# Kernel optimization log

Hardware: AMD Instinct MI355X
Metric: run time of the kernel (lower is better)

Reference implementation:

```python
import jax, jax.numpy as jnp
import numpy as np

BATCH = 16384
NUM_CLASSES = 1000
FEA_DIM = 1024
MARGIN = 5.0


def setup_inputs() -> dict:
    key = jax.random.key(0)
    k1, k2, k3 = jax.random.split(key, 3)
    x = jax.random.normal(k1, (BATCH, FEA_DIM), dtype=jnp.float32)
    labels = jax.random.randint(k2, (BATCH,), 0, NUM_CLASSES)
    centers = jax.random.normal(k3, (NUM_CLASSES, FEA_DIM), dtype=jnp.float32)
    return {"x": x, "labels": labels, "centers": centers}


def reference(x, labels, centers):
    # Half squared euclidean distances via the GEMM expansion:
    # 0.5*||a-b||^2 = 0.5*(||a||^2 + ||b||^2 - 2 a.b)
    B = x.shape[0]
    C = centers.shape[0]
    x2 = jnp.sum(x * x, axis=1, keepdims=True)          # [B,1]
    c2 = jnp.sum(centers * centers, axis=1)             # [C]
    d_xc = 0.5 * (x2 + c2[None, :] - 2.0 * (x @ centers.T))   # [B,C]
    d_cc = 0.5 * (c2[:, None] + c2[None, :] - 2.0 * (centers @ centers.T))  # [C,C]

    is_label = labels[:, None] == jnp.arange(C)[None, :]  # [B,C] bool
    inf = jnp.float32(jnp.inf)

    # pos_center: distance to own class center
    pos = jnp.take_along_axis(d_xc, labels[:, None], axis=1)[:, 0]       # [B]
    # neg_center: min distance to any other class center
    neg = jnp.min(jnp.where(is_label, inf, d_xc), axis=1)                # [B]
    # centers term: min distance between own center and any other center
    cen = jnp.min(jnp.where(is_label, inf, d_cc[labels]), axis=1)        # [B]

    loss = jax.nn.relu(pos + MARGIN - neg) + jax.nn.relu(MARGIN + 2.0 - cen)
    return jnp.sum(loss) / B
```

## Files before the change

### kernel.cpp

```cpp
#include <hip/hip_runtime.h>
#include <hip/hip_bf16.h>
#include <stdint.h>

#define BATCH   16384
#define NCLASS  1000
#define CPAD    1024
#define FDIM    1024
#define MARGINF 5.0f

typedef __attribute__((ext_vector_type(4))) float f32x4;
typedef __attribute__((ext_vector_type(8))) short bf16x8;

#define SB()    __builtin_amdgcn_s_barrier()
#define LGKM0() asm volatile("s_waitcnt lgkmcnt(0)" ::: "memory")
#define VMC4()  asm volatile("s_waitcnt vmcnt(4)" ::: "memory")
#define VMC0()  asm volatile("s_waitcnt vmcnt(0)" ::: "memory")
#define SCH0()  __builtin_amdgcn_sched_barrier(0)

__device__ __forceinline__ void gload16(const void* g, void* l) {
    __builtin_amdgcn_global_load_lds(
        (const __attribute__((address_space(1))) void*)g,
        (__attribute__((address_space(3))) void*)l, 16, 0, 0);
}

__device__ __forceinline__ unsigned short f2bf(float f) {
    __hip_bfloat16 h = __float2bfloat16(f);
    return __builtin_bit_cast(unsigned short, h);
}

__global__ void prep(const float* __restrict__ x, const float* __restrict__ c,
                     unsigned short* __restrict__ xb, unsigned short* __restrict__ cb,
                     float* __restrict__ c2, float* __restrict__ out) {
    const int bid = blockIdx.x;
    const int t   = threadIdx.x;
    if (bid == 0 && t == 0) atomicExch(out, 0.0f);
    if (bid < CPAD) {
        const int k = bid;
        if (k >= NCLASS) {
            ((ushort4*)(cb + (size_t)k * FDIM))[t] = make_ushort4(0, 0, 0, 0);
            if (t == 0) c2[k] = 1e30f;
            return;
        }
        float4 v = ((const float4*)(c + (size_t)k * FDIM))[t];
        ushort4 o;
        o.x = f2bf(v.x); o.y = f2bf(v.y); o.z = f2bf(v.z); o.w = f2bf(v.w);
        ((ushort4*)(cb + (size_t)k * FDIM))[t] = o;
        float ss = v.x * v.x + v.y * v.y + v.z * v.z + v.w * v.w;
        #pragma unroll
        for (int s = 1; s < 64; s <<= 1) ss += __shfl_xor(ss, s, 64);
        __shared__ float sred[4];
        int lane = t & 63, wid = t >> 6;
        if (lane == 0) sred[wid] = ss;
        __syncthreads();
        if (t == 0) c2[k] = sred[0] + sred[1] + sred[2] + sred[3];
    } else {
        int i = (bid - CPAD) * 256 + t;
        const int stride = 2048 * 256;
        #pragma unroll
        for (int it = 0; it < 8; ++it, i += stride) {
            float4 v = ((const float4*)x)[i];
            ushort4 o;
            o.x = f2bf(v.x); o.y = f2bf(v.y); o.z = f2bf(v.z); o.w = f2bf(v.w);
            ((ushort4*)xb)[i] = o;
        }
    }
}

__launch_bounds__(256)
__global__ void cc_gemm(const unsigned short* __restrict__ cb,
                        const float* __restrict__ c2,
                        float* __restrict__ cpmin)
{
    __shared__ __align__(16) char sA[128 * 64 * 2];
    __shared__ __align__(16) char sB[128 * 64 * 2];
    const int bid = blockIdx.x;
    const int bx = bid & 7, by = bid >> 3;
    const int t    = threadIdx.x;
    const int lane = t & 63;
    const int wave = t >> 6;
    const int wrow = wave >> 1, wcol = wave & 1;
    const int lo4  = lane & 15, hi2 = lane >> 4;
    const int rowBase = bx * 128, colBase = by * 128;

    f32x4 acc[4][4];
    #pragma unroll
    for (int m = 0; m < 4; m++)
        #pragma unroll
        for (int n = 0; n < 4; n++) acc[m][n] = (f32x4){0.f, 0.f, 0.f, 0.f};

    const int g_t = t & 7, r_t = t >> 3;
    const unsigned short* ga[4]; const unsigned short* gb[4];
    char* la[4]; char* lb[4];
    #pragma unroll
    for (int cch = 0; cch < 4; ++cch) {
        const int row = cch * 32 + r_t;
        const int sc  = g_t ^ (row & 7);
        ga[cch] = cb + (size_t)(rowBase + row) * FDIM + sc * 8;
        gb[cch] = cb + (size_t)(colBase + row) * FDIM + sc * 8;
        la[cch] = sA + (cch * 256 + (t & 192)) * 16;
        lb[cch] = sB + (cch * 256 + (t & 192)) * 16;
    }
    for (int kt = 0; kt < 16; ++kt) {
        __syncthreads();
        #pragma unroll
        for (int cch = 0; cch < 4; ++cch) {
            gload16(ga[cch], la[cch]);
            gload16(gb[cch], lb[cch]);
            ga[cch] += 64; gb[cch] += 64;
        }
        __syncthreads();
        #pragma unroll
        for (int ks = 0; ks < 2; ++ks) {
            bf16x8 af[4], bfr[4];
            #pragma unroll
            for (int m = 0; m < 4; m++) {
                const int r = wrow * 64 + m * 16 + lo4;
                const int slot = (ks * 4 + hi2) ^ (r & 7);
                af[m] = *(const bf16x8*)(sA + r * 128 + slot * 16);
            }
            #pragma unroll
            for (int n = 0; n < 4; n++) {
                const int r = wcol * 64 + n * 16 + lo4;
                const int slot = (ks * 4 + hi2) ^ (r & 7);
                bfr[n] = *(const bf16x8*)(sB + r * 128 + slot * 16);
            }
            #pragma unroll
            for (int m = 0; m < 4; m++)
                #pragma unroll
                for (int n = 0; n < 4; n++)
                    acc[m][n] = __builtin_amdgcn_mfma_f32_16x16x32_bf16(af[m], bfr[n], acc[m][n], 0, 0, 0);
        }
    }
    __syncthreads();
    float* sPM = (float*)sA;
    float bias[4]; int colg[4];
    #pragma unroll
    for (int n = 0; n < 4; n++) {
        const int col = colBase + wcol * 64 + n * 16 + lo4;
        colg[n] = col;
        bias[n] = 0.5f * c2[col];
    }
    #pragma unroll
    for (int m = 0; m < 4; m++) {
        #pragma unroll
        for (int j = 0; j < 4; j++) {
            const int rloc  = wrow * 64 + m * 16 + hi2 * 4 + j;
            const int rglob = rowBase + rloc;
            float vmin = 1e30f;
            #pragma unroll
            for (int n = 0; n < 4; n++) {
                float tv = acc[m][n][j] + bias[n];
                if (colg[n] == rglob) tv = 1e30f;
                vmin = fminf(vmin, tv);
            }
            vmin = fminf(vmin, __shfl_xor(vmin, 1, 64));
            vmin = fminf(vmin, __shfl_xor(vmin, 2, 64));
            vmin = fminf(vmin, __shfl_xor(vmin, 4, 64));
            vmin = fminf(vmin, __shfl_xor(vmin, 8, 64));
            if (lo4 == 0) sPM[wcol * 128 + rloc] = vmin;
        }
    }
    __syncthreads();
    if (t < 128)
        cpmin[(size_t)(rowBase + t) * 8 + by] = fminf(sPM[t], sPM[128 + t]);
}

__launch_bounds__(512, 2)
__global__ void gemm8(const unsigned short* __restrict__ xb,
                      const unsigned short* __restrict__ cb,
                      const float* __restrict__ c2,
                      const int* __restrict__ labels,
                      float* __restrict__ pmin,
                      float* __restrict__ pos)
{
    __shared__ __align__(16) char L[131072];

    const int bid = blockIdx.x;
    const int tid = (bid & 7) * 32 + (bid >> 3);
    const int bx = tid >> 2, by = tid & 3;
    const int rowBase = bx * 256, colBase = by * 256;

    const int t    = threadIdx.x;
    const int lane = t & 63;
    const int w    = t >> 6;
    const int wrow = w >> 2, wcol = w & 3;
    const int lo4  = lane & 15, hi2 = lane >> 4;
    const int wb   = w << 10;

    const int srow = t >> 2;
    const int g0   = (t & 3) ^ (srow & 3);
    const unsigned short* sApt[2];
    const unsigned short* sBpt[2];
    sApt[0] = xb + (size_t)(rowBase + srow)       * FDIM + g0 * 8;
    sApt[1] = xb + (size_t)(rowBase + 128 + srow) * FDIM + g0 * 8;
    sBpt[0] = cb + (size_t)(colBase + srow)       * FDIM + g0 * 8;
    sBpt[1] = cb + (size_t)(colBase + 128 + srow) * FDIM + g0 * 8;

    auto stage = [&](int ldsOff, const unsigned short* s0, const unsigned short* s1) {
        gload16(s0, L + ldsOff + wb);
        gload16(s1, L + ldsOff + 8192 + wb);
    };

    const int gsw = ((hi2 ^ (lo4 & 3)) << 4);
    auto LDA = [&](int slot, int ks, int m) -> bf16x8 {
        const int r = wrow * 128 + m * 16 + lo4;
        return *(const bf16x8*)(L + slot + ks * 16384 + r * 64 + gsw);
    };
    auto LDB = [&](int slot, int ks, int n) -> bf16x8 {
        const int r = wcol * 64 + n * 16 + lo4;
        return *(const bf16x8*)(L + slot + 32768 + ks * 16384 + r * 64 + gsw);
    };

    f32x4 acc[8][4];
    #pragma unroll
    for (int m = 0; m < 8; m++)
        #pragma unroll
        for (int n = 0; n < 4; n++) acc[m][n] = (f32x4){0.f, 0.f, 0.f, 0.f};

    bf16x8 af[8], b0, b1;

#define MFMA16(N0, N1, B0_, B1_)                                                   \
    __builtin_amdgcn_s_setprio(1);                                                 \
    _Pragma("unroll")                                                              \
    for (int m = 0; m < 8; ++m) {                                                  \
        acc[m][N0] = __builtin_amdgcn_mfma_f32_16x16x32_bf16(af[m], B0_, acc[m][N0], 0, 0, 0); \
        acc[m][N1] = __builtin_amdgcn_mfma_f32_16x16x32_bf16(af[m], B1_, acc[m][N1], 0, 0, 0); \
    }                                                                              \
    __builtin_amdgcn_s_setprio(0);

    stage(0,         sApt[0],      sApt[1]);
    stage(32768,     sBpt[0],      sBpt[1]);
    stage(16384,     sApt[0] + 32, sApt[1] + 32);
    stage(49152,     sBpt[0] + 32, sBpt[1] + 32);
    VMC0();
    SB();

    for (int kt = 0; kt < 15; ++kt) {
        const int slot  = (kt & 1) << 16;
        const int nslot = slot ^ 65536;
        const int nk = (kt + 1) * 64;
        #pragma unroll
        for (int m = 0; m < 8; ++m) af[m] = LDA(slot, 0, m);
        b0 = LDB(slot, 0, 0); b1 = LDB(slot, 0, 1);
        stage(nslot, sApt[0] + nk, sApt[1] + nk);
        SB(); LGKM0(); SCH0();
        MFMA16(0, 1, b0, b1);
        SB();
        b0 = LDB(slot, 0, 2); b1 = LDB(slot, 0, 3);
        stage(nslot + 32768, sBpt[0] + nk, sBpt[1] + nk);
        SB(); LGKM0(); SCH0();
        MFMA16(2, 3, b0, b1);
        VMC4();
        SB();
        #pragma unroll
        for (int m = 0; m < 8; ++m) af[m] = LDA(slot, 1, m);
        b0 = LDB(slot, 1, 0); b1 = LDB(slot, 1, 1);
        stage(nslot + 16384, sApt[0] + nk + 32, sApt[1] + nk + 32);
        SB(); LGKM0(); SCH0();
        MFMA16(0, 1, b0, b1);
        SB();
        b0 = LDB(slot, 1, 2); b1 = LDB(slot, 1, 3);
        stage(nslot + 49152, sBpt[0] + nk + 32, sBpt[1] + nk + 32);
        SB(); LGKM0(); SCH0();
        MFMA16(2, 3, b0, b1);
        VMC4();
        SB();
    }
    {
        const int slot = 65536;
        #pragma unroll
        for (int m = 0; m < 8; ++m) af[m] = LDA(slot, 0, m);
        b0 = LDB(slot, 0, 0); b1 = LDB(slot, 0, 1);
        SB(); LGKM0(); SCH0();
        MFMA16(0, 1, b0, b1);
        SB();
        b0 = LDB(slot, 0, 2); b1 = LDB(slot, 0, 3);
        SB(); LGKM0(); SCH0();
        MFMA16(2, 3, b0, b1);
        VMC0();
        SB();
        #pragma unroll
        for (int m = 0; m < 8; ++m) af[m] = LDA(slot, 1, m);
        b0 = LDB(slot, 1, 0); b1 = LDB(slot, 1, 1);
        SB(); LGKM0(); SCH0();
        MFMA16(0, 1, b0, b1);
        SB();
        b0 = LDB(slot, 1, 2); b1 = LDB(slot, 1, 3);
        SB(); LGKM0(); SCH0();
        MFMA16(2, 3, b0, b1);
        SB();
    }

    float* sPM  = (float*)L;
    int*   sLab = (int*)(L + 4096);
    if (t < 256) sLab[t] = labels[rowBase + t];
    __syncthreads();

    float bias[4]; int colg[4];
    #pragma unroll
    for (int n = 0; n < 4; n++) {
        const int col = colBase + wcol * 64 + n * 16 + lo4;
        colg[n] = col;
        bias[n] = 0.5f * c2[col];
    }
    #pragma unroll
    for (int m = 0; m < 8; m++) {
        #pragma unroll
        for (int j = 0; j < 4; j++) {
            const int rloc  = wrow * 128 + m * 16 + hi2 * 4 + j;
            const int rglob = rowBase + rloc;
            const int lab   = sLab[rloc];
            float vmin = 1e30f;
            #pragma unroll
            for (int n = 0; n < 4; n++) {
                float tv = acc[m][n][j] + bias[n];
                if (colg[n] == lab) {
                    pos[rglob] = tv;
                    tv = 1e30f;
                }
                vmin = fminf(vmin, tv);
            }
            vmin = fminf(vmin, __shfl_xor(vmin, 1, 64));
            vmin = fminf(vmin, __shfl_xor(vmin, 2, 64));
            vmin = fminf(vmin, __shfl_xor(vmin, 4, 64));
            vmin = fminf(vmin, __shfl_xor(vmin, 8, 64));
            if (lo4 == 0) sPM[wcol * 256 + rloc] = vmin;
        }
    }
    __syncthreads();
    if (t < 256) {
        const float v = fminf(fminf(sPM[t], sPM[256 + t]), fminf(sPM[512 + t], sPM[768 + t]));
        pmin[(size_t)(rowBase + t) * 4 + by] = v;
    }
#undef MFMA16
}

__global__ void loss_k(const float* __restrict__ pmin, const float* __restrict__ pos,
                       const int* __restrict__ labels, const float* __restrict__ cpmin,
                       const float* __restrict__ c2, float* __restrict__ out) {
    const int r = blockIdx.x * 256 + threadIdx.x;
    float neg = 1e30f;
    #pragma unroll
    for (int i = 0; i < 4; i++) neg = fminf(neg, pmin[(size_t)r * 4 + i]);
    const int lab = labels[r];
    float cmin = 1e30f;
    #pragma unroll
    for (int i = 0; i < 8; i++) cmin = fminf(cmin, cpmin[(size_t)lab * 8 + i]);
    const float cen = 0.5f * c2[lab] + cmin;
    float v = fmaxf(pos[r] + MARGINF - neg, 0.f) + fmaxf(MARGINF + 2.0f - cen, 0.f);
    #pragma unroll
    for (int s = 1; s < 64; s <<= 1) v += __shfl_xor(v, s, 64);
    __shared__ float sred[4];
    int lane = threadIdx.x & 63, wid = threadIdx.x >> 6;
    if (lane == 0) sred[wid] = v;
    __syncthreads();
    if (threadIdx.x == 0)
        atomicAdd(out, (sred[0] + sred[1] + sred[2] + sred[3]) * (1.0f / (float)BATCH));
}

extern "C" void kernel_launch(void* const* d_in, const int* in_sizes, int n_in,
                              void* d_out, int out_size, void* d_ws, size_t ws_size,
                              hipStream_t stream) {
    const float* x       = (const float*)d_in[0];
    const int*   labels  = (const int*)d_in[1];
    const float* centers = (const float*)d_in[2];
    float* out = (float*)d_out;

    char* ws = (char*)d_ws;
    size_t off = 0;
    unsigned short* xb = (unsigned short*)(ws + off); off += (size_t)BATCH * FDIM * 2;
    unsigned short* cb = (unsigned short*)(ws + off); off += (size_t)CPAD * FDIM * 2;
    float* c2    = (float*)(ws + off); off += (size_t)CPAD * 4;
    float* pmin  = (float*)(ws + off); off += (size_t)BATCH * 4 * 4;
    float* pos   = (float*)(ws + off); off += (size_t)BATCH * 4;
    float* cpmin = (float*)(ws + off); off += (size_t)CPAD * 8 * 4;

    prep<<<dim3(CPAD + 2048), dim3(256), 0, stream>>>(x, centers, xb, cb, c2, out);
    cc_gemm<<<dim3(64), dim3(256), 0, stream>>>(cb, c2, cpmin);
    gemm8<<<dim3(256), dim3(512), 0, stream>>>(xb, cb, c2, labels, pmin, pos);
    loss_k<<<dim3(BATCH / 256), dim3(256), 0, stream>>>(pmin, pos, labels, cpmin, c2, out);
}
```

Baseline: 163.6 us.

## Overlap center-center GEMM with x conversion and change LDS swizzle

Splits the prep kernel so the small centers conversion runs first. The 64-block center-center GEMM then shares a launch with the large x-to-bf16 conversion, so the under-occupying cc_gemm overlaps the bandwidth-bound conversion instead of running serially. It also changes the XOR swizzle pattern for LDS staging and fragment reads in the main GEMM, aiming to reduce bank conflicts. The two swizzle expressions must still match each other, or the GEMM results will be wrong.

```diff
diff --git a/kernel.cpp b/kernel.cpp
--- a/kernel.cpp
+++ b/kernel.cpp
@@ -28,53 +28,35 @@
     return __builtin_bit_cast(unsigned short, h);
 }
 
-__global__ void prep(const float* __restrict__ x, const float* __restrict__ c,
-                     unsigned short* __restrict__ xb, unsigned short* __restrict__ cb,
-                     float* __restrict__ c2, float* __restrict__ out) {
-    const int bid = blockIdx.x;
-    const int t   = threadIdx.x;
-    if (bid == 0 && t == 0) atomicExch(out, 0.0f);
-    if (bid < CPAD) {
-        const int k = bid;
-        if (k >= NCLASS) {
-            ((ushort4*)(cb + (size_t)k * FDIM))[t] = make_ushort4(0, 0, 0, 0);
-            if (t == 0) c2[k] = 1e30f;
-            return;
-        }
-        float4 v = ((const float4*)(c + (size_t)k * FDIM))[t];
-        ushort4 o;
-        o.x = f2bf(v.x); o.y = f2bf(v.y); o.z = f2bf(v.z); o.w = f2bf(v.w);
-        ((ushort4*)(cb + (size_t)k * FDIM))[t] = o;
-        float ss = v.x * v.x + v.y * v.y + v.z * v.z + v.w * v.w;
-        #pragma unroll
-        for (int s = 1; s < 64; s <<= 1) ss += __shfl_xor(ss, s, 64);
-        __shared__ float sred[4];
-        int lane = t & 63, wid = t >> 6;
-        if (lane == 0) sred[wid] = ss;
-        __syncthreads();
-        if (t == 0) c2[k] = sred[0] + sred[1] + sred[2] + sred[3];
-    } else {
-        int i = (bid - CPAD) * 256 + t;
-        const int stride = 2048 * 256;
-        #pragma unroll
-        for (int it = 0; it < 8; ++it, i += stride) {
-            float4 v = ((const float4*)x)[i];
-            ushort4 o;
-            o.x = f2bf(v.x); o.y = f2bf(v.y); o.z = f2bf(v.z); o.w = f2bf(v.w);
-            ((ushort4*)xb)[i] = o;
-        }
-    }
-}
-
-__launch_bounds__(256)
-__global__ void cc_gemm(const unsigned short* __restrict__ cb,
-                        const float* __restrict__ c2,
-                        float* __restrict__ cpmin)
+__global__ void prep_c(const float* __restrict__ c, unsigned short* __restrict__ cb,
+                       float* __restrict__ c2, float* __restrict__ out) {
+    const int k = blockIdx.x;
+    const int t = threadIdx.x;
+    if (k == 0 && t == 0) atomicExch(out, 0.0f);
+    if (k >= NCLASS) {
+        ((ushort4*)(cb + (size_t)k * FDIM))[t] = make_ushort4(0, 0, 0, 0);
+        if (t == 0) c2[k] = 1e30f;
+        return;
+    }
+    float4 v = ((const float4*)(c + (size_t)k * FDIM))[t];
+    ushort4 o;
+    o.x = f2bf(v.x); o.y = f2bf(v.y); o.z = f2bf(v.z); o.w = f2bf(v.w);
+    ((ushort4*)(cb + (size_t)k * FDIM))[t] = o;
+    float ss = v.x * v.x + v.y * v.y + v.z * v.z + v.w * v.w;
+    #pragma unroll
+    for (int s = 1; s < 64; s <<= 1) ss += __shfl_xor(ss, s, 64);
+    __shared__ float sred[4];
+    int lane = t & 63, wid = t >> 6;
+    if (lane == 0) sred[wid] = ss;
+    __syncthreads();
+    if (t == 0) c2[k] = sred[0] + sred[1] + sred[2] + sred[3];
+}
+
+__device__ __forceinline__ void cc_tile(const unsigned short* __restrict__ cb,
+                                        const float* __restrict__ c2,
+                                        float* __restrict__ cpmin,
+                                        int bx, int by, char* sA, char* sB)
 {
-    __shared__ __align__(16) char sA[128 * 64 * 2];
-    __shared__ __align__(16) char sB[128 * 64 * 2];
-    const int bid = blockIdx.x;
-    const int bx = bid & 7, by = bid >> 3;
     const int t    = threadIdx.x;
     const int lane = t & 63;
     const int wave = t >> 6;
@@ -165,6 +147,27 @@
         cpmin[(size_t)(rowBase + t) * 8 + by] = fminf(sPM[t], sPM[128 + t]);
 }
 
+__global__ void prepx_cc(const float* __restrict__ x, unsigned short* __restrict__ xb,
+                         const unsigned short* __restrict__ cb,
+                         const float* __restrict__ c2, float* __restrict__ cpmin) {
+    __shared__ __align__(16) char sA[128 * 64 * 2];
+    __shared__ __align__(16) char sB[128 * 64 * 2];
+    const int bid = blockIdx.x;
+    if (bid < 64) {
+        cc_tile(cb, c2, cpmin, bid & 7, bid >> 3, sA, sB);
+    } else {
+        int i = (bid - 64) * 256 + threadIdx.x;
+        const int stride = 2048 * 256;
+        #pragma unroll
+        for (int it = 0; it < 8; ++it, i += stride) {
+            float4 v = ((const float4*)x)[i];
+            ushort4 o;
+            o.x = f2bf(v.x); o.y = f2bf(v.y); o.z = f2bf(v.z); o.w = f2bf(v.w);
+            ((ushort4*)xb)[i] = o;
+        }
+    }
+}
+
 __launch_bounds__(512, 2)
 __global__ void gemm8(const unsigned short* __restrict__ xb,
                       const unsigned short* __restrict__ cb,
@@ -188,7 +191,7 @@
     const int wb   = w << 10;
 
     const int srow = t >> 2;
-    const int g0   = (t & 3) ^ (srow & 3);
+    const int g0   = (t & 3) ^ ((t >> 3) & 3);
     const unsigned short* sApt[2];
     const unsigned short* sBpt[2];
     sApt[0] = xb + (size_t)(rowBase + srow)       * FDIM + g0 * 8;
@@ -201,7 +204,7 @@
         gload16(s1, L + ldsOff + 8192 + wb);
     };
 
-    const int gsw = ((hi2 ^ (lo4 & 3)) << 4);
+    const int gsw = ((hi2 ^ ((lo4 >> 1) & 3)) << 4);
     auto LDA = [&](int slot, int ks, int m) -> bf16x8 {
         const int r = wrow * 128 + m * 16 + lo4;
         return *(const bf16x8*)(L + slot + ks * 16384 + r * 64 + gsw);
@@ -375,8 +378,8 @@
     float* pos   = (float*)(ws + off); off += (size_t)BATCH * 4;
     float* cpmin = (float*)(ws + off); off += (size_t)CPAD * 8 * 4;
 
-    prep<<<dim3(CPAD + 2048), dim3(256), 0, stream>>>(x, centers, xb, cb, c2, out);
-    cc_gemm<<<dim3(64), dim3(256), 0, stream>>>(cb, c2, cpmin);
+    prep_c<<<dim3(CPAD), dim3(256), 0, stream>>>(centers, cb, c2, out);
+    prepx_cc<<<dim3(64 + 2048), dim3(256), 0, stream>>>(x, xb, cb, c2, cpmin);
     gemm8<<<dim3(256), dim3(512), 0, stream>>>(xb, cb, c2, labels, pmin, pos);
     loss_k<<<dim3(BATCH / 256), dim3(256), 0, stream>>>(pmin, pos, labels, cpmin, c2, out);
 }
```

New measurement: 162.6 us. About the same (-0.6%).
